# Kernel optimization log

Measured on AMD Instinct MI355X. Metric: run time of the kernel, lower is better.

The kernel has to match this reference:

```python
import jax, jax.numpy as jnp
import numpy as np

ALPHA, BETA, LAMB, GAMMA = 1.0, 1.0, 1e-4, 1.0
K_NN, TAU = 50, 0.1
EPS = 1e-8


def _sqdist(A, B):
    # ||a - b||^2, clamped at 0 like the torch code
    d2 = (A * A).sum(1)[:, None] + (B * B).sum(1)[None, :] - 2.0 * (A @ B.T)
    return jnp.maximum(d2, 0.0)


def _mmd(s, t):
    comb = jnp.concatenate([s, t], axis=0)
    sigma_sq = jax.lax.stop_gradient(jnp.median(_sqdist(comb, comb))) / 2.0
    sigma_sq = jnp.where(sigma_sq < 1e-6, jnp.float32(1.0), sigma_sq)
    g = 1.0 / (sigma_sq + EPS)
    kxx = jnp.exp(-g * _sqdist(s, s)).mean()
    kyy = jnp.exp(-g * _sqdist(t, t)).mean()
    kxy = jnp.exp(-g * _sqdist(s, t)).mean()
    return jnp.maximum(kxx + kyy - 2.0 * kxy, 0.0)


def setup_inputs() -> dict:
    key = jax.random.key(0)
    ks = jax.random.split(key, 8)
    B, d, N, Nq, K = 256, 128, 200000, 10000, K_NN
    q_batch = jax.random.normal(ks[0], (B, d), jnp.float32)
    X = jax.random.normal(ks[1], (N, d), jnp.float32)
    W = jax.random.normal(ks[2], (d, d), jnp.float32) * (1.0 / np.sqrt(d))
    b = jnp.zeros((d,), jnp.float32)
    pre_weights = jax.random.uniform(ks[3], (Nq, K), jnp.float32)
    pre_weights = pre_weights / pre_weights.sum(1, keepdims=True)
    pre_indices = jax.random.randint(ks[4], (Nq, K), 0, N)
    q_indices = jax.random.randint(ks[5], (B,), 0, Nq)
    idx = jax.random.randint(ks[6], (B,), 0, N)
    return {"q_batch": q_batch, "X": X, "W": W, "b": b,
            "pre_weights": pre_weights, "pre_indices": pre_indices,
            "q_indices": q_indices, "idx": idx}


def reference(q_batch, X, W, b, pre_weights, pre_indices, q_indices, idx):
    Tq = q_batch @ W.T + b                                   # model(q_batch), Linear(d, d)
    # ---- MMD between mapped queries and a random database batch ----
    loss_dist = _mmd(Tq, X[idx])
    # ---- exact KNN (faiss IndexFlatL2 equivalent) on detached embeddings ----
    d2_all = _sqdist(jax.lax.stop_gradient(Tq), X)           # [B, N]
    _, post_idx = jax.lax.top_k(-d2_all, K_NN)               # [B, K] nearest neighbors
    Xn = X[post_idx]                                         # [B, K, d]
    l2 = ((Tq[:, None, :] - Xn) ** 2).sum(-1)                # [B, K] (grad flows here)
    post_w = jax.nn.softmax(-l2 / TAU, axis=1)
    # ---- union-KL, vectorized over batch (exact torch.unique semantics) ----
    pre_i = pre_indices[q_indices]                           # [B, K]
    pre_w = pre_weights[q_indices]                           # [B, K]
    cat = jnp.concatenate([pre_i, post_idx], axis=1)         # [B, 2K]
    # multiplicity of each id within the concatenated list -> collapse duplicates
    mult = (cat[:, :, None] == cat[:, None, :]).sum(-1).astype(jnp.float32)  # [B, 2K]
    p_raw = jnp.einsum('bmk,bk->bm',
                       (cat[:, :, None] == pre_i[:, None, :]).astype(jnp.float32), pre_w)
    q_raw = jnp.einsum('bmk,bk->bm',
                       (cat[:, :, None] == post_idx[:, None, :]).astype(jnp.float32), post_w)
    p_c = jnp.maximum(p_raw, EPS)
    q_c = jnp.maximum(q_raw, EPS)
    p = p_c / (p_c / mult).sum(1, keepdims=True)             # normalize over union
    q = q_c / (q_c / mult).sum(1, keepdims=True)
    kl = ((p * (jnp.log(p) - jnp.log(q))) / mult).sum(1)     # KL(p || q) per sample
    loss_knn = kl.mean()
    # ---- L2 regularization of model params & anchor loss ----
    loss_reg = 0.5 * ((W ** 2).sum() + (b ** 2).sum())
    loss_anchor = ((Tq - q_batch) ** 2).sum(1).mean()
    total = ALPHA * loss_dist + BETA * loss_knn + LAMB * loss_reg + GAMMA * loss_anchor
    return jnp.stack([total, loss_dist, loss_knn, loss_anchor])
```

## Files before the change

kernel.cpp:

```cpp
#include <hip/hip_runtime.h>
#include <cstdint>

#define D 128
#define NPTS 200000
#define KNN 50
#define CAP 8192
#define NS 8192
#define SLACK 2.0f
#define BAND 4.0f
#define EB 2048

#define OFF_ACC    0
#define OFF_SEL    256
#define OFF_CNT    1024
#define OFF_HIST0  17408
#define OFF_HIST12 148480
#define ZERO_BYTES 214016
#define OFF_COMB   214016
#define OFF_D2     476160
#define OFF_XN     1524736
#define OFF_SAMP   2324736
#define OFF_EBUF   2324736
#define OFF_THR    10713344
#define OFF_CANDI  10714368
#define OFF_SCO    19102976
#define OFF_TQSW   27491584
#define OFF_XBF    27557120
#define OFF_ANCP   78757120
#define OFF_WREGP  78758144
#define OFF_BCNT   78758400
#define OFF_KSA    78774272

typedef __attribute__((ext_vector_type(8))) short bf16x8;
typedef __attribute__((ext_vector_type(4))) float f32x4;
typedef const __attribute__((address_space(1))) void* gas_p;
typedef __attribute__((address_space(3))) void* las_p;

__device__ __forceinline__ unsigned fkey(float f) {
    unsigned u = __float_as_uint(f);
    return u ^ ((unsigned)((int)u >> 31) | 0x80000000u);
}

__device__ __forceinline__ void stage8k(const unsigned short* __restrict__ g,
                                        unsigned short* l, int w, int lane)
{
    #pragma unroll
    for (int j = 0; j < 2; j++) {
        const unsigned short* gp = g + j * 2048 + w * 512 + lane * 8;
        unsigned short* lp = l + j * 2048 + w * 512;
        __builtin_amdgcn_global_load_lds((gas_p)gp, (las_p)lp, 16, 0, 0);
    }
}

__global__ void k_phase1(const float* __restrict__ q, const float* __restrict__ X,
                         const float* __restrict__ W, const float* __restrict__ bb,
                         const int* __restrict__ idx, float* __restrict__ comb,
                         unsigned short* __restrict__ tqsw, unsigned short* __restrict__ xbf,
                         float* __restrict__ xn, float* __restrict__ ancp,
                         float* __restrict__ wregp, float* __restrict__ wszero)
{
    const int blk = blockIdx.x, t = threadIdx.x;
    if (blk < 12500) {
        __shared__ float xr4[4][16];
        const int lr = t & 15;
        const float4* src = (const float4*)(X + ((long)(blk * 16 + lr)) * D + (t >> 4) * 8);
        float4 v0 = src[0], v1 = src[1];
        uint4 pk;
        pk.x = (__float_as_uint(v0.x) >> 16) | (__float_as_uint(v0.y) & 0xFFFF0000u);
        pk.y = (__float_as_uint(v0.z) >> 16) | (__float_as_uint(v0.w) & 0xFFFF0000u);
        pk.z = (__float_as_uint(v1.x) >> 16) | (__float_as_uint(v1.y) & 0xFFFF0000u);
        pk.w = (__float_as_uint(v1.z) >> 16) | (__float_as_uint(v1.w) & 0xFFFF0000u);
        *(uint4*)(xbf + (long)blk * 2048 + t * 8) = pk;
        float ssq = v0.x*v0.x + v0.y*v0.y + v0.z*v0.z + v0.w*v0.w
                  + v1.x*v1.x + v1.y*v1.y + v1.z*v1.z + v1.w*v1.w;
        ssq += __shfl_down(ssq, 32);
        ssq += __shfl_down(ssq, 16);
        if ((t & 63) < 16) xr4[t >> 6][lr] = ssq;
        __syncthreads();
        if (t < 16) xn[blk * 16 + t] = xr4[0][t] + xr4[1][t] + xr4[2][t] + xr4[3][t];
    } else if (blk < 12628) {
        __shared__ float rowv[2][D];
        __shared__ float red[2][D];
        const int half = t >> 7, tt = t & 127;
        const int row = (blk - 12500) * 2 + half;
        rowv[half][tt] = q[row * D + tt];
        __syncthreads();
        float s = 0.f;
        const float* wr = W + tt * D;
        #pragma unroll 4
        for (int k = 0; k < D; k++) s = fmaf(rowv[half][k], wr[k], s);
        s += bb[tt];
        comb[row * D + tt] = s;
        unsigned ub = __float_as_uint(s);
        unsigned short hv = (unsigned short)((ub + 0x7fffu + ((ub >> 16) & 1u)) >> 16);
        int ksb = tt >> 5, quad = (tt & 31) >> 3, jj = tt & 7;
        int lane = quad * 16 + (row & 15);
        tqsw[(row >> 4) * 2048 + ksb * 512 + lane * 8 + jj] = hv;
        float dd = s - rowv[half][tt];
        red[half][tt] = dd * dd;
        __syncthreads();
        for (int off = 64; off > 0; off >>= 1) { if (tt < off) red[half][tt] += red[half][tt + off]; __syncthreads(); }
        if (tt == 0) ancp[row] = red[half][0];
    } else if (blk < 12756) {
        const int half = t >> 7, tt = t & 127;
        const int i = (blk - 12628) * 2 + half;
        comb[(256 + i) * D + tt] = X[(long)idx[i] * D + tt];
    } else if (blk < 12760) {
        __shared__ float wred[4];
        const int base = (blk - 12756) * 4096;
        float s = 0.f;
        #pragma unroll 4
        for (int k = 0; k < 16; k++) { float v = W[base + k * 256 + t]; s = fmaf(v, v, s); }
        if (blk == 12756 && t < D) { float v = bb[t]; s = fmaf(v, v, s); }
        #pragma unroll
        for (int off = 32; off > 0; off >>= 1) s += __shfl_down(s, off);
        if ((t & 63) == 0) wred[t >> 6] = s;
        __syncthreads();
        if (t == 0) wregp[blk - 12756] = wred[0] + wred[1] + wred[2] + wred[3];
    } else {
        uint4* z = (uint4*)wszero;
        const uint4 zz = make_uint4(0u, 0u, 0u, 0u);
        for (int i = (blk - 12760) * 256 + t; i < (ZERO_BYTES / 16); i += 1024) z[i] = zz;
    }
}

__global__ void k_d2m(const float* __restrict__ comb, float* __restrict__ D2w,
                      unsigned* __restrict__ hist0, const unsigned short* __restrict__ tqsw,
                      const unsigned short* __restrict__ xbf, const float* __restrict__ xn,
                      float* __restrict__ samp)
{
    __shared__ __align__(16) char smraw[51456];
    const int b = blockIdx.x, t = threadIdx.x;
    if (b < 1024) {
        float (*cj)[D + 1] = (float(*)[D + 1])smraw;
        float (*ci)[D]     = (float(*)[D])(smraw + 33024);
        unsigned* h        = (unsigned*)(smraw + 35072);
        const int ib = b >> 3, jb = b & 7;
        const int w = t >> 6, l = t & 63;
        for (int m = t; m < 4096; m += 256) h[m] = 0;
        const int irow = ib * 4 + w;
        ci[w][l] = comb[irow * D + l];
        ci[w][l + 64] = comb[irow * D + l + 64];
        const float4* src = (const float4*)(comb + (jb * 64) * D);
        #pragma unroll
        for (int m = 0; m < 8; m++) {
            int u = m * 256 + t;
            int r = u >> 5, c = u & 31;
            float4 v = src[u];
            cj[r][c * 4 + 0] = v.x; cj[r][c * 4 + 1] = v.y; cj[r][c * 4 + 2] = v.z; cj[r][c * 4 + 3] = v.w;
        }
        __syncthreads();
        float s = 0.f;
        #pragma unroll 4
        for (int k = 0; k < D; k++) { float d = ci[w][k] - cj[l][k]; s = fmaf(d, d, s); }
        D2w[irow * 512 + jb * 64 + l] = s;
        atomicAdd(&h[__float_as_uint(s) >> 20], 1u);
        __syncthreads();
        const int sh = (ib + jb) & 7;
        for (int m = t; m < 4096; m += 256) { unsigned v = h[m]; if (v) atomicAdd(&hist0[m * 8 + sh], v); }
    } else {
        unsigned short* sb = (unsigned short*)smraw;
        const int w = t >> 6, lane = t & 63;
        const int lr = lane & 15, quad = lane >> 4;
        const int ck = b - 1024;
        stage8k(xbf + (long)ck * 4096, sb, w, lane);
        bf16x8 a[4][4];
        #pragma unroll
        for (int i = 0; i < 4; i++)
            #pragma unroll
            for (int ks = 0; ks < 4; ks++)
                a[i][ks] = *(const bf16x8*)(tqsw + (w * 4 + i) * 2048 + ks * 512 + lane * 8);
        __syncthreads();
        #pragma unroll
        for (int tt = 0; tt < 2; tt++) {
            const int r = (ck * 2 + tt) * 16 + lr;
            float xnv = xn[r];
            bf16x8 bfr[4];
            #pragma unroll
            for (int ks = 0; ks < 4; ks++)
                bfr[ks] = *(const bf16x8*)(sb + tt * 2048 + ks * 512 + lane * 8);
            f32x4 acc4[4];
            #pragma unroll
            for (int i = 0; i < 4; i++) acc4[i] = (f32x4){0.f, 0.f, 0.f, 0.f};
            #pragma unroll
            for (int ks = 0; ks < 4; ks++)
                #pragma unroll
                for (int i = 0; i < 4; i++)
                    acc4[i] = __builtin_amdgcn_mfma_f32_16x16x32_bf16(a[i][ks], bfr[ks], acc4[i], 0, 0, 0);
            #pragma unroll
            for (int i = 0; i < 4; i++)
                #pragma unroll
                for (int reg = 0; reg < 4; reg++) {
                    int qq = w * 64 + i * 16 + quad * 4 + reg;
                    samp[qq * NS + r] = xnv - 2.f * acc4[i][reg];
                }
        }
    }
}

__global__ void k_h1thr(const float* __restrict__ D2w, unsigned* __restrict__ hist12,
                        const unsigned* __restrict__ hist0, unsigned* __restrict__ sel,
                        const float* __restrict__ samp, float* __restrict__ thr)
{
    __shared__ unsigned buf[8192];
    __shared__ unsigned bins[4096];
    __shared__ unsigned part[256];
    __shared__ unsigned selll[4];
    __shared__ unsigned wred[4];
    const int t = threadIdx.x;
    if (blockIdx.x < 256) {
        unsigned s = 0;
        #pragma unroll
        for (int m = 0; m < 16; m++) {
            int bin = t * 16 + m;
            unsigned bs = 0;
            #pragma unroll
            for (int sh = 0; sh < 8; sh++) bs += hist0[bin * 8 + sh];
            bins[bin] = bs;
            s += bs;
        }
        part[t] = s;
        for (int m = t; m < 8192; m += 256) buf[m] = 0;
        __syncthreads();
        if (t == 0) {
            for (int tg = 0; tg < 2; tg++) {
                unsigned r = tg ? 131072u : 131071u;
                int c = 0;
                while (part[c] <= r) { r -= part[c]; c++; }
                int b = c * 16;
                while (bins[b] <= r) { r -= bins[b]; b++; }
                selll[2 * tg] = (unsigned)b; selll[2 * tg + 1] = r;
            }
            if (blockIdx.x == 0) {
                sel[0] = selll[0]; sel[1] = selll[1]; sel[2] = selll[2]; sel[3] = selll[3];
            }
        }
        __syncthreads();
        unsigned p0 = selll[0], p1 = selll[2];
        const int e0 = blockIdx.x * 1024;
        for (int m = 0; m < 4; m++) {
            unsigned key = __float_as_uint(D2w[e0 + m * 256 + t]);
            if ((key >> 20) == p0) atomicAdd(&buf[(key >> 8) & 0xFFFu], 1u);
            if ((key >> 20) == p1) atomicAdd(&buf[4096 + ((key >> 8) & 0xFFFu)], 1u);
        }
        __syncthreads();
        for (int m = t; m < 8192; m += 256) { unsigned v = buf[m]; if (v) atomicAdd(&hist12[m], v); }
    } else {
        const int q = blockIdx.x - 256;
        unsigned kreg[32];
        #pragma unroll
        for (int i = 0; i < 32; i++) kreg[i] = fkey(samp[q * NS + i * 256 + t]);
        unsigned v = 0;
        for (int bit = 31; bit >= 0; bit--) {
            unsigned trial = v | (1u << bit);
            unsigned c = 0;
            #pragma unroll
            for (int i = 0; i < 32; i++) c += (kreg[i] < trial) ? 1u : 0u;
            #pragma unroll
            for (int off = 32; off > 0; off >>= 1) c += __shfl_down(c, off);
            if ((t & 63) == 0) wred[t >> 6] = c;
            __syncthreads();
            unsigned total = wred[0] + wred[1] + wred[2] + wred[3];
            __syncthreads();
            if (total <= (unsigned)(KNN - 1)) v = trial;
        }
        if (t == 0) {
            unsigned orig = (v & 0x80000000u) ? (v ^ 0x80000000u) : ~v;
            thr[q] = __uint_as_float(orig) + SLACK;
        }
    }
}

#define FILT_BODY(SBUF)                                                              \
    do {                                                                             \
        _Pragma("unroll")                                                            \
        for (int tt = 0; tt < 2; tt++) {                                             \
            const int r = (ck * 2 + tt) * 16 + lr;                                   \
            float xnv = xn[r];                                                       \
            bf16x8 bv[4];                                                            \
            _Pragma("unroll")                                                        \
            for (int ks2 = 0; ks2 < 4; ks2++)                                        \
                bv[ks2] = *(const bf16x8*)(SBUF + tt * 2048 + ks2 * 512 + lane * 8); \
            f32x4 acc4[4];                                                           \
            _Pragma("unroll")                                                        \
            for (int i = 0; i < 4; i++) acc4[i] = (f32x4){0.f, 0.f, 0.f, 0.f};       \
            _Pragma("unroll")                                                        \
            for (int ks2 = 0; ks2 < 4; ks2++)                                        \
                _Pragma("unroll")                                                    \
                for (int i = 0; i < 4; i++)                                          \
                    acc4[i] = __builtin_amdgcn_mfma_f32_16x16x32_bf16(a[i][ks2], bv[ks2], acc4[i], 0, 0, 0); \
            _Pragma("unroll")                                                        \
            for (int i = 0; i < 4; i++)                                              \
                _Pragma("unroll")                                                    \
                for (int reg = 0; reg < 4; reg++) {                                  \
                    float s = xnv - 2.f * acc4[i][reg];                              \
                    if (s <= th_r[i][reg]) {                                         \
                        unsigned qq = (unsigned)(w * 64 + i * 16 + quad * 4 + reg);  \
                        unsigned p = atomicAdd(&lcnt, 1u);                           \
                        if (p < 1024u) { lbuf[p] = (qq << 18) | (unsigned)r; lsco[p] = fkey(s); } \
                        else {                                                       \
                            unsigned dd2 = gbase + p;                                \
                            if (dd2 < EB) { eb[dd2] = (qq << 18) | (unsigned)r; ebs[dd2] = fkey(s); } \
                        }                                                            \
                    }                                                                \
                }                                                                    \
        }                                                                            \
    } while (0)

__global__ __launch_bounds__(256) void k_filt2(const unsigned short* __restrict__ tqsw,
    const unsigned short* __restrict__ xbf, const float* __restrict__ xn,
    const float* __restrict__ thr, unsigned* __restrict__ ebuf, unsigned* __restrict__ esco,
    unsigned* __restrict__ bcnt, const float* __restrict__ D2w,
    unsigned* __restrict__ hist12, unsigned* __restrict__ sel)
{
    if (blockIdx.x >= 1024) {
        __shared__ unsigned h2c[512];
        __shared__ unsigned part2[256];
        __shared__ unsigned pfx[2];
        __shared__ unsigned rr[2];
        const int t = threadIdx.x;
        for (int tg = 0; tg < 2; tg++) {
            const unsigned* hh = hist12 + tg * 4096;
            unsigned s = 0;
            for (int m = 0; m < 16; m++) s += hh[t * 16 + m];
            part2[t] = s;
            __syncthreads();
            if (t == 0) {
                unsigned r = sel[1 + 2 * tg];
                int c = 0;
                while (part2[c] <= r) { r -= part2[c]; c++; }
                int b = c * 16;
                while (hh[b] <= r) { r -= hh[b]; b++; }
                pfx[tg] = (sel[2 * tg] << 12) | (unsigned)b;
                rr[tg] = r;
            }
            __syncthreads();
        }
        if (blockIdx.x == 1024 && t == 0) {
            sel[4] = pfx[0]; sel[5] = rr[0]; sel[6] = pfx[1]; sel[7] = rr[1];
        }
        h2c[t] = 0; h2c[256 + t] = 0;
        __syncthreads();
        unsigned p0 = pfx[0], p1 = pfx[1];
        const int e0 = (blockIdx.x - 1024) * 1024;
        for (int m = 0; m < 4; m++) {
            unsigned key = __float_as_uint(D2w[e0 + m * 256 + t]);
            if ((key >> 8) == p0) atomicAdd(&h2c[key & 0xFFu], 1u);
            if ((key >> 8) == p1) atomicAdd(&h2c[256 + (key & 0xFFu)], 1u);
        }
        __syncthreads();
        unsigned* gp = hist12 + 8192;
        unsigned v0 = h2c[t], v1 = h2c[256 + t];
        if (v0) atomicAdd(&gp[t], v0);
        if (v1) atomicAdd(&gp[4096 + t], v1);
        return;
    }
    __shared__ unsigned short sbA[4096];
    __shared__ unsigned short sbB[4096];
    __shared__ unsigned lbuf[1024];
    __shared__ unsigned lsco[1024];
    __shared__ unsigned lcnt;
    __shared__ unsigned gbase;
    const int t = threadIdx.x;
    const int w = t >> 6, lane = t & 63;
    const int lr = lane & 15, quad = lane >> 4;
    unsigned* eb  = ebuf + (unsigned)blockIdx.x * EB;
    unsigned* ebs = esco + (unsigned)blockIdx.x * EB;
    bf16x8 a[4][4];
    #pragma unroll
    for (int i = 0; i < 4; i++)
        #pragma unroll
        for (int ks = 0; ks < 4; ks++)
            a[i][ks] = *(const bf16x8*)(tqsw + (w * 4 + i) * 2048 + ks * 512 + lane * 8);
    float th_r[4][4];
    #pragma unroll
    for (int i = 0; i < 4; i++)
        #pragma unroll
        for (int reg = 0; reg < 4; reg++)
            th_r[i][reg] = thr[w * 64 + i * 16 + quad * 4 + reg];
    int ck = blockIdx.x;
    bool phaseA = true;
    if (t == 0) { lcnt = 0; gbase = 0; }
    stage8k(xbf + (long)ck * 4096, sbA, w, lane);
    __syncthreads();
    while (true) {
        const int ckn = ck + 1024;
        const bool has = ckn < 6250;
        if (phaseA) {
            if (has) stage8k(xbf + (long)ckn * 4096, sbB, w, lane);
            FILT_BODY(sbA);
        } else {
            if (has) stage8k(xbf + (long)ckn * 4096, sbA, w, lane);
            FILT_BODY(sbB);
        }
        __syncthreads();
        unsigned n = lcnt;
        if (!has || n >= 512u) {
            unsigned nf = (n < 1024u) ? n : 1024u;
            unsigned gb = gbase;
            for (unsigned m = t; m < nf; m += 256) {
                unsigned d = gb + m;
                if (d < EB) { eb[d] = lbuf[m]; ebs[d] = lsco[m]; }
            }
            __syncthreads();
            if (t == 0) { gbase = gb + n; lcnt = 0; }
            __syncthreads();
        }
        if (!has) break;
        ck = ckn; phaseA = !phaseA;
    }
    if (t == 0) bcnt[blockIdx.x] = (gbase < EB) ? gbase : EB;
}

__global__ __launch_bounds__(256) void k_scatmmd(const unsigned* __restrict__ ebuf,
    const unsigned* __restrict__ esco, const unsigned* __restrict__ bcnt,
    int* __restrict__ cand_i, unsigned* __restrict__ ksa, unsigned* __restrict__ cnt,
    const float* __restrict__ D2w, const unsigned* __restrict__ hist12,
    const unsigned* __restrict__ sel, float* __restrict__ acc)
{
    const int t = threadIdx.x;
    if (blockIdx.x >= 128) {
        __shared__ unsigned h2[512];
        __shared__ float gsh;
        __shared__ float part[12];
        const int w = t >> 6;
        h2[t] = hist12[8192 + t];
        h2[256 + t] = hist12[8192 + 4096 + t];
        __syncthreads();
        if (t == 0) {
            unsigned key[2];
            for (int tg = 0; tg < 2; tg++) {
                unsigned r = sel[5 + 2 * tg];
                const unsigned* hh = h2 + tg * 256;
                int b = 0;
                while (hh[b] <= r) { r -= hh[b]; b++; }
                key[tg] = (sel[4 + 2 * tg] << 8) | (unsigned)b;
            }
            float med = 0.5f * (__uint_as_float(key[0]) + __uint_as_float(key[1]));
            float ssq = 0.5f * med;
            if (ssq < 1e-6f) ssq = 1.0f;
            gsh = 1.0f / (ssq + 1e-8f);
        }
        __syncthreads();
        const float g = gsh;
        float s[3] = {0.f, 0.f, 0.f};
        const int e0 = (blockIdx.x - 128) * 1024;
        #pragma unroll
        for (int m = 0; m < 4; m++) {
            int e = e0 + m * 256 + t;
            int i = e >> 9, j = e & 511;
            float v = expf(-g * D2w[e]);
            int qd = (i < 256) ? ((j < 256) ? 0 : 2) : ((j < 256) ? 2 : 1);
            s[qd] += v;
        }
        #pragma unroll
        for (int c = 0; c < 3; c++) {
            float x = s[c];
            #pragma unroll
            for (int off = 32; off > 0; off >>= 1) x += __shfl_down(x, off);
            if ((t & 63) == 0) part[w * 3 + c] = x;
        }
        __syncthreads();
        if (t == 0)
            for (int c = 0; c < 3; c++)
                atomicAdd(&acc[2 + c], part[c] + part[3 + c] + part[6 + c] + part[9 + c]);
        return;
    }
    __shared__ unsigned hist[256];
    __shared__ unsigned startp[256];
    const int b0 = blockIdx.x * 8;
    hist[t] = 0;
    __syncthreads();
    for (int b = b0; b < b0 + 8; b++) {
        unsigned n = bcnt[b];
        const unsigned* e = ebuf + (unsigned)b * EB;
        for (unsigned m = t; m < n; m += 256)
            atomicAdd(&hist[e[m] >> 18], 1u);
    }
    __syncthreads();
    unsigned c = hist[t];
    if (c) {
        unsigned base = atomicAdd(&cnt[t * 16], c);
        startp[t] = ((unsigned)t << 13) + base;
    }
    __syncthreads();
    for (int b = b0; b < b0 + 8; b++) {
        unsigned n = bcnt[b];
        const unsigned* e = ebuf + (unsigned)b * EB;
        const unsigned* e2 = esco + (unsigned)b * EB;
        for (unsigned m = t; m < n; m += 256) {
            unsigned ent = e[m];
            unsigned sk = e2[m];
            unsigned qq = ent >> 18;
            unsigned pos = atomicAdd(&startp[qq], 1u);
            if (pos < ((qq + 1u) << 13)) { cand_i[pos] = (int)(ent & 0x3FFFFu); ksa[pos] = sk; }
        }
    }
}

__global__ __launch_bounds__(1024) void k_rp(const float* __restrict__ comb,
                        const float* __restrict__ X,
                        const int* __restrict__ cand_i, const unsigned* __restrict__ ksa,
                        const unsigned* __restrict__ cnt,
                        const int* __restrict__ pri,
                        const float* __restrict__ prw, const int* __restrict__ qix,
                        const float* __restrict__ xn,
                        float* __restrict__ acc, unsigned* __restrict__ sel,
                        const float* __restrict__ ancp, const float* __restrict__ wregp,
                        float* __restrict__ out)
{
    __shared__ unsigned ks[CAP];
    __shared__ int sidx[2048];
    __shared__ unsigned eks[2048];
    __shared__ float qrow[D];
    __shared__ unsigned wred[16];
    __shared__ unsigned scnt, wpos, eqn;
    __shared__ int eq[64];
    __shared__ int pidx[KNN];
    __shared__ float l2s[KNN];
    __shared__ float pw[KNN];
    __shared__ int ci[100];
    __shared__ float pwv[50], qwv[50];
    __shared__ float pterm[100], qterm[100], kterm[100];
    __shared__ float Sp, Sq;
    const int q = blockIdx.x, t = threadIdx.x;
    if (t < D) qrow[t] = comb[q * D + t];
    if (t == 0) { wpos = 0; eqn = 0; scnt = 0; }
    unsigned nn = cnt[q * 16];
    const int n = (nn < (unsigned)CAP) ? (int)nn : CAP;
    for (int m = t; m < n; m += 1024) ks[m] = ksa[q * CAP + m];
    __syncthreads();
    unsigned kregA[8];
    #pragma unroll
    for (int i = 0; i < 8; i++) {
        int m = i * 1024 + t;
        kregA[i] = (m < n) ? ks[m] : 0xFFFFFFFFu;
    }
    int kk = KNN - 1; if (kk > n - 1) kk = n - 1;
    unsigned va = 0;
    for (int bit = 31; bit >= 0; bit--) {
        unsigned trial = va | (1u << bit);
        unsigned c = 0;
        #pragma unroll
        for (int i = 0; i < 8; i++) c += (kregA[i] < trial) ? 1u : 0u;
        #pragma unroll
        for (int off = 32; off > 0; off >>= 1) c += __shfl_down(c, off);
        if ((t & 63) == 0) wred[t >> 6] = c;
        __syncthreads();
        unsigned total = 0;
        #pragma unroll
        for (int i = 0; i < 16; i++) total += wred[i];
        __syncthreads();
        if (total <= (unsigned)kk) va = trial;
    }
    unsigned ovaf = (va & 0x80000000u) ? (va ^ 0x80000000u) : ~va;
    unsigned vkeep = fkey(__uint_as_float(ovaf) + BAND);
    for (int m = t; m < n; m += 1024) {
        if (ks[m] <= vkeep) {
            unsigned p = atomicAdd(&scnt, 1u);
            if (p < 2048u) sidx[p] = cand_i[q * CAP + m];
        }
    }
    __syncthreads();
    const bool cpath = (scnt <= 2048u);
    const int ns = cpath ? (int)scnt : n;
    const int g = t >> 3, j = t & 7;
    if (cpath) {
        for (int m = g; m < ns; m += 128) {
            int r = sidx[m];
            const float4* xr = (const float4*)(X + (long)r * D);
            float s = 0.f;
            #pragma unroll
            for (int p = 0; p < 4; p++) {
                float4 xv = xr[j * 4 + p];
                float4 qv = *(const float4*)&qrow[(j * 4 + p) * 4];
                s = fmaf(xv.x, qv.x, fmaf(xv.y, qv.y, fmaf(xv.z, qv.z, fmaf(xv.w, qv.w, s))));
            }
            s += __shfl_down(s, 4); s += __shfl_down(s, 2); s += __shfl_down(s, 1);
            if (j == 0) eks[m] = fkey(xn[r] - 2.f * s);
        }
    } else {
        for (int m = g; m < ns; m += 128) {
            int r = cand_i[q * CAP + m];
            const float4* xr = (const float4*)(X + (long)r * D);
            float s = 0.f;
            #pragma unroll
            for (int p = 0; p < 4; p++) {
                float4 xv = xr[j * 4 + p];
                float4 qv = *(const float4*)&qrow[(j * 4 + p) * 4];
                s = fmaf(xv.x, qv.x, fmaf(xv.y, qv.y, fmaf(xv.z, qv.z, fmaf(xv.w, qv.w, s))));
            }
            s += __shfl_down(s, 4); s += __shfl_down(s, 2); s += __shfl_down(s, 1);
            if (j == 0) ks[m] = fkey(xn[r] - 2.f * s);
        }
    }
    __syncthreads();
    kk = KNN - 1; if (kk > ns - 1) kk = ns - 1;
    unsigned v = 0;
    for (int bit = 31; bit >= 0; bit--) {
        unsigned trial = v | (1u << bit);
        unsigned c = 0;
        for (int m = t; m < ns; m += 1024) {
            unsigned kv = cpath ? eks[m] : ks[m];
            c += (kv < trial) ? 1u : 0u;
        }
        #pragma unroll
        for (int off = 32; off > 0; off >>= 1) c += __shfl_down(c, off);
        if ((t & 63) == 0) wred[t >> 6] = c;
        __syncthreads();
        unsigned total = 0;
        #pragma unroll
        for (int i = 0; i < 16; i++) total += wred[i];
        __syncthreads();
        if (total <= (unsigned)kk) v = trial;
    }
    for (int m = t; m < ns; m += 1024) {
        unsigned kv = cpath ? eks[m] : ks[m];
        int r = cpath ? sidx[m] : cand_i[q * CAP + m];
        if (kv < v) {
            unsigned p = atomicAdd(&wpos, 1u);
            pidx[p] = r;
        } else if (kv == v) {
            unsigned p = atomicAdd(&eqn, 1u);
            if (p < 64) eq[p] = r;
        }
    }
    __syncthreads();
    if (t == 0) {
        int c1 = (int)wpos, need = KNN - c1;
        int ne = (eqn < 64u) ? (int)eqn : 64;
        for (int a = 0; a < ne; a++)
            for (int b2 = a + 1; b2 < ne; b2++)
                if (eq[b2] < eq[a]) { int tmp = eq[a]; eq[a] = eq[b2]; eq[b2] = tmp; }
        for (int a = 0; a < need && a < ne; a++) pidx[c1 + a] = eq[a];
    }
    __syncthreads();
    for (int nb = g; nb < KNN; nb += 128) {
        long r = pidx[nb];
        const float4* xr = (const float4*)(X + r * D);
        float s = 0.f;
        #pragma unroll
        for (int p = 0; p < 4; p++) {
            float4 xv = xr[j * 4 + p];
            float4 qv = *(const float4*)&qrow[(j * 4 + p) * 4];
            float d0 = qv.x - xv.x, d1 = qv.y - xv.y, d2 = qv.z - xv.z, d3 = qv.w - xv.w;
            s += d0 * d0 + d1 * d1 + d2 * d2 + d3 * d3;
        }
        s += __shfl_down(s, 4); s += __shfl_down(s, 2); s += __shfl_down(s, 1);
        if (j == 0) l2s[nb] = s;
    }
    int qi = qix[q];
    if (t >= 128 && t < 178) { int k = t - 128; ci[k] = pri[qi * 50 + k]; pwv[k] = prw[qi * 50 + k]; }
    __syncthreads();
    if (t < 64) {
        float logit = (t < KNN) ? (-l2s[t] * 10.0f) : -3.4e38f;
        float m = logit;
        #pragma unroll
        for (int off = 32; off > 0; off >>= 1) m = fmaxf(m, __shfl_down(m, off));
        m = __shfl(m, 0);
        float e = (t < KNN) ? expf(logit - m) : 0.f;
        float ss = e;
        #pragma unroll
        for (int off = 32; off > 0; off >>= 1) ss += __shfl_down(ss, off);
        ss = __shfl(ss, 0);
        if (t < KNN) pw[t] = e / ss;
    }
    __syncthreads();
    if (t < 50) { ci[50 + t] = pidx[t]; qwv[t] = pw[t]; }
    __syncthreads();
    float pc = 0.f, qc = 0.f, mult = 0.f;
    if (t < 100) {
        int c = ci[t];
        float pr = 0.f, qr = 0.f;
        for (int k = 0; k < 50; k++) {
            bool m1 = (c == ci[k]); bool m2 = (c == ci[50 + k]);
            mult += (m1 ? 1.f : 0.f) + (m2 ? 1.f : 0.f);
            pr += m1 ? pwv[k] : 0.f;
            qr += m2 ? qwv[k] : 0.f;
        }
        pc = fmaxf(pr, 1e-8f); qc = fmaxf(qr, 1e-8f);
        pterm[t] = pc / mult; qterm[t] = qc / mult;
    }
    __syncthreads();
    if (t == 0) { float a = 0.f, b2 = 0.f; for (int m = 0; m < 100; m++) { a += pterm[m]; b2 += qterm[m]; } Sp = a; Sq = b2; }
    __syncthreads();
    if (t < 100) {
        float p = pc / Sp, qq2 = qc / Sq;
        kterm[t] = (p * (logf(p) - logf(qq2))) / mult;
    }
    __syncthreads();
    if (t == 0) {
        float s = 0.f;
        for (int m = 0; m < 100; m++) s += kterm[m];
        atomicAdd(&acc[1], s);
        __threadfence();
        unsigned old = atomicAdd(&sel[15], 1u);
        if (old == 255u) {
            __threadfence();
            float lknn = atomicAdd(&acc[1], 0.f) / 256.f;
            float reg = 0.f;
            #pragma unroll
            for (int m = 0; m < 4; m++) reg += wregp[m];
            reg *= 0.5f;
            float anc = 0.f;
            for (int m = 0; m < 256; m++) anc += ancp[m];
            float lanc = anc / 256.f;
            float kxx = acc[2] / 65536.f, kyy = acc[3] / 65536.f, kxy = acc[4] / 131072.f;
            float ld = fmaxf(kxx + kyy - 2.f * kxy, 0.f);
            out[0] = ld + lknn + 1e-4f * reg + lanc;
            out[1] = ld; out[2] = lknn; out[3] = lanc;
        }
    }
}

extern "C" void kernel_launch(void* const* d_in, const int* in_sizes, int n_in,
                              void* d_out, int out_size, void* d_ws, size_t ws_size,
                              hipStream_t stream)
{
    (void)in_sizes; (void)n_in; (void)out_size; (void)ws_size;
    const float* q   = (const float*)d_in[0];
    const float* X   = (const float*)d_in[1];
    const float* W   = (const float*)d_in[2];
    const float* bb  = (const float*)d_in[3];
    const float* prw = (const float*)d_in[4];
    const int*   pri = (const int*)d_in[5];
    const int*   qix = (const int*)d_in[6];
    const int*   idx = (const int*)d_in[7];
    float* out = (float*)d_out;
    char* ws = (char*)d_ws;
    float*    acc   = (float*)(ws + OFF_ACC);
    unsigned* sel   = (unsigned*)(ws + OFF_SEL);
    unsigned* cnt   = (unsigned*)(ws + OFF_CNT);
    unsigned* hist0 = (unsigned*)(ws + OFF_HIST0);
    unsigned* hist12= (unsigned*)(ws + OFF_HIST12);
    float*    comb  = (float*)(ws + OFF_COMB);
    float*    D2w   = (float*)(ws + OFF_D2);
    float*    xn    = (float*)(ws + OFF_XN);
    float*    samp  = (float*)(ws + OFF_SAMP);
    float*    thr   = (float*)(ws + OFF_THR);
    int*      cix   = (int*)(ws + OFF_CANDI);
    unsigned* ebuf  = (unsigned*)(ws + OFF_EBUF);
    unsigned* esco  = (unsigned*)(ws + OFF_SCO);
    unsigned* bcnt  = (unsigned*)(ws + OFF_BCNT);
    unsigned* ksa   = (unsigned*)(ws + OFF_KSA);
    unsigned short* tqsw = (unsigned short*)(ws + OFF_TQSW);
    unsigned short* xbf  = (unsigned short*)(ws + OFF_XBF);
    float*    ancp  = (float*)(ws + OFF_ANCP);
    float*    wregp = (float*)(ws + OFF_WREGP);

    hipLaunchKernelGGL(k_phase1,  dim3(12764),   dim3(256), 0, stream, q, X, W, bb, idx, comb, tqsw, xbf, xn, ancp, wregp, acc);
    hipLaunchKernelGGL(k_d2m,     dim3(1280),    dim3(256), 0, stream, comb, D2w, hist0, tqsw, xbf, xn, samp);
    hipLaunchKernelGGL(k_h1thr,   dim3(512),     dim3(256), 0, stream, D2w, hist12, hist0, sel, samp, thr);
    hipLaunchKernelGGL(k_filt2,   dim3(1280),    dim3(256), 0, stream, tqsw, xbf, xn, thr, ebuf, esco, bcnt, D2w, hist12, sel);
    hipLaunchKernelGGL(k_scatmmd, dim3(384),     dim3(256), 0, stream, ebuf, esco, bcnt, cix, ksa, cnt, D2w, hist12, sel, acc);
    hipLaunchKernelGGL(k_rp,      dim3(256),     dim3(1024), 0, stream, comb, X, cix, ksa, cnt, pri, prw, qix, xn, acc, sel, ancp, wregp, out);
}
```

Baseline: 360.2 us.

## Replace block-wide radix selects with histogram threshold and single-wave select

In the rerank kernel, the first 32-pass bitwise radix select, which synchronizes the whole block twice per bit, is replaced by a 4096-bin shared histogram on the top 12 key bits. A prefix scan over that histogram locates the bin holding the k-th key, and the keep threshold is taken from that bin's upper edge plus the band. The second exact select now runs in one wavefront using xor-shuffles, so it needs no block barriers. The histogram buffer is reused for sidx/eks to save LDS. The coarser threshold may keep more candidates, which could push more queries onto the slow non-compact path, and single-wave selection serializes work when ns is large.

Result: faster. 336.7 us (-6.5%).

```diff
diff --git a/kernel.cpp b/kernel.cpp
--- a/kernel.cpp
+++ b/kernel.cpp
@@ -510,11 +510,10 @@
                         float* __restrict__ out)
 {
     __shared__ unsigned ks[CAP];
-    __shared__ int sidx[2048];
-    __shared__ unsigned eks[2048];
+    __shared__ unsigned hs[4096];
+    __shared__ unsigned wsum[16];
     __shared__ float qrow[D];
-    __shared__ unsigned wred[16];
-    __shared__ unsigned scnt, wpos, eqn;
+    __shared__ unsigned scnt, wpos, eqn, bsel, vsh;
     __shared__ int eq[64];
     __shared__ int pidx[KNN];
     __shared__ float l2s[KNN];
@@ -525,36 +524,56 @@
     __shared__ float Sp, Sq;
     const int q = blockIdx.x, t = threadIdx.x;
     if (t < D) qrow[t] = comb[q * D + t];
-    if (t == 0) { wpos = 0; eqn = 0; scnt = 0; }
+    if (t == 0) { wpos = 0; eqn = 0; scnt = 0; bsel = 4095u; }
     unsigned nn = cnt[q * 16];
     const int n = (nn < (unsigned)CAP) ? (int)nn : CAP;
-    for (int m = t; m < n; m += 1024) ks[m] = ksa[q * CAP + m];
-    __syncthreads();
-    unsigned kregA[8];
-    #pragma unroll
-    for (int i = 0; i < 8; i++) {
-        int m = i * 1024 + t;
-        kregA[i] = (m < n) ? ks[m] : 0xFFFFFFFFu;
-    }
+    for (int m = t; m < 4096; m += 1024) hs[m] = 0;
+    __syncthreads();
+    for (int m = t; m < n; m += 1024) {
+        unsigned kv = ksa[q * CAP + m];
+        ks[m] = kv;
+        atomicAdd(&hs[kv >> 20], 1u);
+    }
+    __syncthreads();
     int kk = KNN - 1; if (kk > n - 1) kk = n - 1;
-    unsigned va = 0;
-    for (int bit = 31; bit >= 0; bit--) {
-        unsigned trial = va | (1u << bit);
-        unsigned c = 0;
-        #pragma unroll
-        for (int i = 0; i < 8; i++) c += (kregA[i] < trial) ? 1u : 0u;
-        #pragma unroll
-        for (int off = 32; off > 0; off >>= 1) c += __shfl_down(c, off);
-        if ((t & 63) == 0) wred[t >> 6] = c;
-        __syncthreads();
-        unsigned total = 0;
-        #pragma unroll
-        for (int i = 0; i < 16; i++) total += wred[i];
-        __syncthreads();
-        if (total <= (unsigned)kk) va = trial;
-    }
-    unsigned ovaf = (va & 0x80000000u) ? (va ^ 0x80000000u) : ~va;
-    unsigned vkeep = fkey(__uint_as_float(ovaf) + BAND);
+    {
+        unsigned h0 = hs[t * 4], h1 = hs[t * 4 + 1], h2 = hs[t * 4 + 2], h3 = hs[t * 4 + 3];
+        unsigned c4 = h0 + h1 + h2 + h3;
+        unsigned sc = c4;
+        #pragma unroll
+        for (int off = 1; off < 64; off <<= 1) {
+            unsigned o = __shfl_up(sc, off);
+            if ((t & 63) >= off) sc += o;
+        }
+        if ((t & 63) == 63) wsum[t >> 6] = sc;
+        __syncthreads();
+        unsigned wbase = 0;
+        #pragma unroll
+        for (int i = 0; i < 16; i++) wbase += (i < (t >> 6)) ? wsum[i] : 0u;
+        unsigned excl = wbase + sc - c4;
+        unsigned kku = (unsigned)kk;
+        if (c4 > 0 && kku >= excl && kku < excl + c4) {
+            unsigned cum = excl;
+            int b = t * 4;
+            if (kku >= cum + h0) { cum += h0; b++;
+                if (kku >= cum + h1) { cum += h1; b++;
+                    if (kku >= cum + h2) { cum += h2; b++; } } }
+            bsel = (unsigned)b;
+        }
+    }
+    __syncthreads();
+    unsigned vkeep;
+    {
+        unsigned b = bsel;
+        if (b >= 4095u) vkeep = 0xFFFFFFFFu;
+        else {
+            unsigned bk = (b + 1u) << 20;
+            unsigned bf = (bk & 0x80000000u) ? (bk ^ 0x80000000u) : ~bk;
+            vkeep = fkey(__uint_as_float(bf) + BAND);
+        }
+    }
+    int* sidx = (int*)hs;
+    unsigned* eks = hs + 2048;
     for (int m = t; m < n; m += 1024) {
         if (ks[m] <= vkeep) {
             unsigned p = atomicAdd(&scnt, 1u);
@@ -595,25 +614,24 @@
         }
     }
     __syncthreads();
-    kk = KNN - 1; if (kk > ns - 1) kk = ns - 1;
-    unsigned v = 0;
-    for (int bit = 31; bit >= 0; bit--) {
-        unsigned trial = v | (1u << bit);
-        unsigned c = 0;
-        for (int m = t; m < ns; m += 1024) {
-            unsigned kv = cpath ? eks[m] : ks[m];
-            c += (kv < trial) ? 1u : 0u;
-        }
-        #pragma unroll
-        for (int off = 32; off > 0; off >>= 1) c += __shfl_down(c, off);
-        if ((t & 63) == 0) wred[t >> 6] = c;
-        __syncthreads();
-        unsigned total = 0;
-        #pragma unroll
-        for (int i = 0; i < 16; i++) total += wred[i];
-        __syncthreads();
-        if (total <= (unsigned)kk) v = trial;
-    }
+    int kk2 = KNN - 1; if (kk2 > ns - 1) kk2 = ns - 1;
+    if (t < 64) {
+        unsigned v = 0;
+        for (int bit = 31; bit >= 0; bit--) {
+            unsigned trial = v | (1u << bit);
+            unsigned c = 0;
+            for (int m = t; m < ns; m += 64) {
+                unsigned kv2 = cpath ? eks[m] : ks[m];
+                c += (kv2 < trial) ? 1u : 0u;
+            }
+            #pragma unroll
+            for (int off = 32; off > 0; off >>= 1) c += __shfl_xor(c, off);
+            if (c <= (unsigned)kk2) v = trial;
+        }
+        if (t == 0) vsh = v;
+    }
+    __syncthreads();
+    const unsigned v = vsh;
     for (int m = t; m < ns; m += 1024) {
         unsigned kv = cpath ? eks[m] : ks[m];
         int r = cpath ? sidx[m] : cand_i[q * CAP + m];
```
